# Performance work log

Hardware: AMD Instinct MI355X
Metric: run time of the kernel (lower is better)

## Reference

```python
import jax, jax.numpy as jnp
import numpy as np

N_NODES = 500000
N_EDGES = 4000000
IN_DIM = 2
HID = 8
N_ITERS = 3


def _edge_net(x, row, col, e1_w, e1_b, e2_w, e2_b):
    # bi = x[col], bo = x[row]; B = cat([bi, bo]) is detached in torch
    B = jax.lax.stop_gradient(jnp.concatenate([x[col], x[row]], axis=-1))  # [E, 2*F]
    h = jnp.tanh(B @ e1_w + e1_b)
    return jax.nn.sigmoid(h @ e2_w + e2_b)  # [E, 1]


def _node_net(x, row, col, edge_attr, n1_w, n1_b, n2_w, n2_b):
    e = jax.lax.stop_gradient(edge_attr)  # [E, 1], detached in torch
    bi = x[col] * e  # [E, F]
    bo = x[row] * e
    mi = jax.ops.segment_sum(bo, col, num_segments=N_NODES)  # scatter_add over col
    mo = jax.ops.segment_sum(bi, row, num_segments=N_NODES)  # scatter_add over row
    M = jax.lax.stop_gradient(jnp.concatenate([mi, mo, x], axis=-1))  # [N, 3*F]
    h = jnp.tanh(M @ n1_w + n1_b)
    return jnp.tanh(h @ n2_w + n2_b)  # [N, HID]


def setup_inputs() -> dict:
    key = jax.random.key(0)
    ks = jax.random.split(key, 12)
    F = IN_DIM + HID  # 10
    s = lambda fan_in: 1.0 / np.sqrt(fan_in)
    return {
        "x": jax.random.normal(ks[0], (N_NODES, IN_DIM), jnp.float32),
        "edge_index": jax.random.randint(ks[1], (2, N_EDGES), 0, N_NODES),
        "win_w": jax.random.uniform(ks[2], (IN_DIM, HID), jnp.float32, -s(IN_DIM), s(IN_DIM)),
        "win_b": jax.random.uniform(ks[3], (HID,), jnp.float32, -s(IN_DIM), s(IN_DIM)),
        "e1_w": jax.random.uniform(ks[4], (2 * F, HID), jnp.float32, -s(2 * F), s(2 * F)),
        "e1_b": jax.random.uniform(ks[5], (HID,), jnp.float32, -s(2 * F), s(2 * F)),
        "e2_w": jax.random.uniform(ks[6], (HID, 1), jnp.float32, -s(HID), s(HID)),
        "e2_b": jax.random.uniform(ks[7], (1,), jnp.float32, -s(HID), s(HID)),
        "n1_w": jax.random.uniform(ks[8], (3 * F, HID), jnp.float32, -s(3 * F), s(3 * F)),
        "n1_b": jax.random.uniform(ks[9], (HID,), jnp.float32, -s(3 * F), s(3 * F)),
        "n2_w": jax.random.uniform(ks[10], (HID, HID), jnp.float32, -s(HID), s(HID)),
        "n2_b": jax.random.uniform(ks[11], (HID,), jnp.float32, -s(HID), s(HID)),
    }


def reference(x, edge_index, win_w, win_b, e1_w, e1_b, e2_w, e2_b, n1_w, n1_b, n2_w, n2_b):
    row, col = edge_index[0], edge_index[1]
    X = x
    H = jnp.tanh(X @ win_w + win_b)  # input_network
    xcat = jnp.concatenate([H, X], axis=-1)  # [N, 10]
    for _ in range(N_ITERS):
        e = _edge_net(xcat, row, col, e1_w, e1_b, e2_w, e2_b)
        H = _node_net(xcat, row, col, e, n1_w, n1_b, n2_w, n2_b)
        xcat = jnp.concatenate([H, X], axis=-1)
    out = _edge_net(xcat, row, col, e1_w, e1_b, e2_w, e2_b)
    return out.squeeze(-1)  # [E]
```

## Files before the change

### kernel.cpp

```cpp
#include <hip/hip_runtime.h>
#include <hip/hip_fp16.h>
#include <math.h>

#define N_NODES 500000
#define N_EDGES 4000000
#define FDIM 10
#define HID 8

#define DSPACE (2 * N_NODES)
#define NB 512
#define BSHIFT 11
#define BMASK 2047
#define NB_USED ((DSPACE + BMASK) / 2048)

#define IN_BLOCKS ((N_NODES + 255) / 256)
#define ROWS_PAD (IN_BLOCKS * 256)
#define NODE_BLOCKS2 ((N_NODES + 127) / 128)

typedef _Float16 h2v __attribute__((ext_vector_type(2)));

__device__ __forceinline__ h2v u2h(unsigned x) {
    union { unsigned u; h2v h; } t; t.u = x; return t.h;
}
__device__ __forceinline__ unsigned packh2(float a, float b) {
    union { __half2 h; unsigned u; } t; t.h = __floats2half2_rn(a, b); return t.u;
}
__device__ __forceinline__ float rfl_f(float x) {
    return __int_as_float(__builtin_amdgcn_readfirstlane(__float_as_int(x)));
}
__device__ __forceinline__ unsigned rfl_u(unsigned x) {
    return (unsigned)__builtin_amdgcn_readfirstlane((int)x);
}

__device__ __forceinline__ int nt_ld_i(const int* p) { return __builtin_nontemporal_load(p); }

__device__ __forceinline__ float fast_tanh(float x) {
    float e = __builtin_amdgcn_exp2f(x * 2.885390082f);
    return 1.0f - 2.0f * __builtin_amdgcn_rcpf(e + 1.0f);
}
__device__ __forceinline__ float fast_sigmoid(float x) {
    float e = __builtin_amdgcn_exp2f(-1.442695041f * x);
    return __builtin_amdgcn_rcpf(1.0f + e);
}

__global__ __launch_bounds__(256) void input_kernel(const float* __restrict__ x,
                                                    const float* __restrict__ win_w,
                                                    const float* __restrict__ win_b,
                                                    uint4* __restrict__ xh,
                                                    unsigned* __restrict__ xs) {
    int n = blockIdx.x * 256 + threadIdx.x;
    float x0 = 0.f, x1 = 0.f;
    if (n < N_NODES) { x0 = x[2 * n]; x1 = x[2 * n + 1]; }
    float h[HID];
#pragma unroll
    for (int j = 0; j < HID; j++)
        h[j] = fast_tanh(x0 * win_w[j] + x1 * win_w[HID + j] + win_b[j]);
    xh[n] = make_uint4(packh2(h[0], h[1]), packh2(h[2], h[3]),
                       packh2(h[4], h[5]), packh2(h[6], h[7]));
    xs[n] = packh2(x0, x1);
}

__global__ void bucket_hist_kernel(const int* __restrict__ row,
                                   const int* __restrict__ col,
                                   int* __restrict__ g_cnt) {
    __shared__ int s_cnt[NB];
    int tid = threadIdx.x;
    for (int i = tid; i < NB; i += 256) s_cnt[i] = 0;
    __syncthreads();
    int base = blockIdx.x * 4096;
#pragma unroll
    for (int k = 0; k < 16; k++) {
        int e = base + k * 256 + tid;
        if (e < N_EDGES) {
            int c = nt_ld_i(col + e), r = nt_ld_i(row + e);
            atomicAdd(&s_cnt[(2 * c) >> BSHIFT], 1);
            atomicAdd(&s_cnt[(2 * r + 1) >> BSHIFT], 1);
        }
    }
    __syncthreads();
    for (int i = tid; i < NB; i += 256) {
        int v = s_cnt[i];
        if (v) atomicAdd(&g_cnt[i], v);
    }
}

__global__ void bucket_scan_kernel(const int* __restrict__ g_cnt,
                                   int* __restrict__ bucket_base,
                                   int* __restrict__ bucket_cur) {
    __shared__ int s[NB];
    int t = threadIdx.x;
    int c = g_cnt[t];
    s[t] = c;
    __syncthreads();
    for (int off = 1; off < NB; off <<= 1) {
        int v = (t >= off) ? s[t - off] : 0;
        __syncthreads();
        s[t] += v;
        __syncthreads();
    }
    int ex = s[t] - c;
    bucket_base[t] = ex;
    bucket_cur[t] = ex;
    if (t == NB - 1) bucket_base[NB] = s[t];
}

__global__ void bin_kernel(const int* __restrict__ row,
                           const int* __restrict__ col,
                           int* __restrict__ bucket_cur,
                           unsigned int* __restrict__ binned) {
    __shared__ int s_cnt[NB];
    __shared__ int s_start[NB];
    __shared__ int s_cur[NB];
    __shared__ int s_gbase[NB];
    __shared__ unsigned int s_items[8192];
    __shared__ unsigned short s_ibkt[8192];

    int tid = threadIdx.x;
    if (tid < NB) s_cnt[tid] = 0;
    __syncthreads();

    int base = blockIdx.x * 4096;
    int cc[4], rr[4];
#pragma unroll
    for (int k = 0; k < 4; k++) {
        int e = base + k * 1024 + tid;
        bool ok = (e < N_EDGES);
        cc[k] = ok ? nt_ld_i(col + e) : -1;
        rr[k] = ok ? nt_ld_i(row + e) : -1;
        if (ok) {
            atomicAdd(&s_cnt[(2 * cc[k]) >> BSHIFT], 1);
            atomicAdd(&s_cnt[(2 * rr[k] + 1) >> BSHIFT], 1);
        }
    }
    __syncthreads();

    if (tid < NB) s_start[tid] = s_cnt[tid];
    __syncthreads();
    for (int off = 1; off < NB; off <<= 1) {
        int v = 0;
        if (tid < NB && tid >= off) v = s_start[tid - off];
        __syncthreads();
        if (tid < NB) s_start[tid] += v;
        __syncthreads();
    }
    if (tid < NB) {
        int ex = s_start[tid] - s_cnt[tid];
        s_start[tid] = ex;
        s_cur[tid] = ex;
    }
    __syncthreads();

#pragma unroll
    for (int k = 0; k < 4; k++) {
        if (cc[k] >= 0) {
            int d0 = 2 * cc[k];
            int b0 = d0 >> BSHIFT;
            int s0 = atomicAdd(&s_cur[b0], 1);
            s_items[s0] = ((unsigned)(d0 & BMASK) << 19) | (unsigned)rr[k];
            s_ibkt[s0] = (unsigned short)b0;
            int d1 = 2 * rr[k] + 1;
            int b1 = d1 >> BSHIFT;
            int s1 = atomicAdd(&s_cur[b1], 1);
            s_items[s1] = ((unsigned)(d1 & BMASK) << 19) | (unsigned)cc[k];
            s_ibkt[s1] = (unsigned short)b1;
        }
    }
    __syncthreads();

    if (tid < NB) s_gbase[tid] = atomicAdd(&bucket_cur[tid], s_cnt[tid]);
    __syncthreads();

    int tot = s_start[NB - 1] + s_cnt[NB - 1];
    for (int s = tid; s < tot; s += 1024) {
        int b = s_ibkt[s];
        int g = s_gbase[b] + (s - s_start[b]);
        binned[g] = s_items[s];
    }
}

__global__ void csr_kernel(const unsigned int* __restrict__ binned,
                           const int* __restrict__ bucket_base,
                           int* __restrict__ offs,
                           int* __restrict__ entries) {
    __shared__ int s_deg[2048];
    __shared__ int s_cur[2048];
    __shared__ int s_pair[1024];

    int t = threadIdx.x;
    int b = blockIdx.x;
    if (b == 0 && t == 0) offs[DSPACE] = 2 * N_EDGES;

    int ebase = bucket_base[b];
    int eend = bucket_base[b + 1];

    s_deg[t] = 0;
    s_deg[t + 1024] = 0;
    __syncthreads();

    for (int p = ebase + t; p < eend; p += 1024)
        atomicAdd(&s_deg[binned[p] >> 19], 1);
    __syncthreads();

    int d0 = s_deg[2 * t], d1 = s_deg[2 * t + 1];
    s_pair[t] = d0 + d1;
    __syncthreads();
    for (int off = 1; off < 1024; off <<= 1) {
        int v = (t >= off) ? s_pair[t - off] : 0;
        __syncthreads();
        s_pair[t] += v;
        __syncthreads();
    }
    int pex = s_pair[t] - (d0 + d1);
    s_cur[2 * t] = pex;
    s_cur[2 * t + 1] = pex + d0;

    int dest0 = b * 2048 + 2 * t;
    if (dest0 < DSPACE) offs[dest0] = ebase + pex;
    if (dest0 + 1 < DSPACE) offs[dest0 + 1] = ebase + pex + d0;
    __syncthreads();

    for (int p = ebase + t; p < eend; p += 1024) {
        unsigned int it = binned[p];
        int dl = it >> 19;
        int other = it & 0x7FFFF;
        int pos = atomicAdd(&s_cur[dl], 1);
        entries[ebase + pos] = other;
    }
}

__global__ __launch_bounds__(256, 6) void node_kernel(
        const uint4* __restrict__ xh,
        const unsigned* __restrict__ xs,
        const int* __restrict__ offs,
        const int* __restrict__ entries,
        const float* __restrict__ e1_w,
        const float* __restrict__ e1_b,
        const float* __restrict__ e2_w,
        const float* __restrict__ e2_b,
        const float* __restrict__ n1_w,
        const float* __restrict__ n1_b,
        const float* __restrict__ n2_w,
        const float* __restrict__ n2_b,
        uint4* __restrict__ xh_next) {
    __shared__ uint4 s_wtop4[10];
    __shared__ uint4 s_wbot4[10];
    __shared__ float s_scal[17];
    __shared__ float s_n1w[30 * HID];
    __shared__ float s_n1b[HID];
    __shared__ float s_n2w[HID * HID];
    __shared__ float s_n2b[HID];
    __shared__ float s_mo[128 * 11];

    int tid = threadIdx.x;
    if (tid < 40) {
        int kk = tid >> 3, j = tid & 7;
        ((unsigned*)s_wtop4)[tid] = packh2(e1_w[(2 * kk) * HID + j],
                                           e1_w[(2 * kk + 1) * HID + j]);
        ((unsigned*)s_wbot4)[tid] = packh2(e1_w[(FDIM + 2 * kk) * HID + j],
                                           e1_w[(FDIM + 2 * kk + 1) * HID + j]);
    } else if (tid < 48) s_scal[tid - 40] = e1_b[tid - 40];
    else if (tid < 56) s_scal[tid - 40] = e2_w[tid - 48];
    else if (tid == 56) s_scal[16] = e2_b[0];
    if (tid < 240) s_n1w[tid] = n1_w[tid];
    else if (tid < 248) s_n1b[tid - 240] = n1_b[tid - 240];
    if (tid < 64) s_n2w[tid] = n2_w[tid];
    else if (tid < 72) s_n2b[tid - 64] = n2_b[tid - 64];
    __syncthreads();

    bool up = tid >= 128;
    int lt = up ? tid - 128 : tid;
    int n = blockIdx.x * 128 + lt;
    bool act = n < N_NODES;

    const uint4* selfw4 = up ? s_wbot4 : s_wtop4;
    const unsigned* othw = up ? (const unsigned*)s_wtop4 : (const unsigned*)s_wbot4;

    unsigned so[40];
#pragma unroll
    for (int i = 0; i < 40; i++) so[i] = rfl_u(othw[i]);
    float sb[HID], sv[HID];
#pragma unroll
    for (int j = 0; j < HID; j++) { sb[j] = rfl_f(s_scal[j]); sv[j] = rfl_f(s_scal[8 + j]); }
    float sc = rfl_f(s_scal[16]);

    unsigned xp[5] = {0, 0, 0, 0, 0};
    float m[FDIM];
#pragma unroll
    for (int k = 0; k < FDIM; k++) m[k] = 0.f;

    if (act) {
        uint4 xq = xh[n]; unsigned xx = xs[n];
        xp[0] = xq.x; xp[1] = xq.y; xp[2] = xq.z; xp[3] = xq.w; xp[4] = xx;

        float us[HID];
#pragma unroll
        for (int j = 0; j < HID; j++) us[j] = sb[j];
#pragma unroll
        for (int kk = 0; kk < 5; kk++) {
            uint4 wa = selfw4[2 * kk];
            uint4 wb = selfw4[2 * kk + 1];
            h2v a = u2h(xp[kk]);
            us[0] = __builtin_amdgcn_fdot2(a, u2h(wa.x), us[0], false);
            us[1] = __builtin_amdgcn_fdot2(a, u2h(wa.y), us[1], false);
            us[2] = __builtin_amdgcn_fdot2(a, u2h(wa.z), us[2], false);
            us[3] = __builtin_amdgcn_fdot2(a, u2h(wa.w), us[3], false);
            us[4] = __builtin_amdgcn_fdot2(a, u2h(wb.x), us[4], false);
            us[5] = __builtin_amdgcn_fdot2(a, u2h(wb.y), us[5], false);
            us[6] = __builtin_amdgcn_fdot2(a, u2h(wb.z), us[6], false);
            us[7] = __builtin_amdgcn_fdot2(a, u2h(wb.w), us[7], false);
        }

        int dest = 2 * n + (up ? 1 : 0);
        int p0 = nt_ld_i(offs + dest), p1 = nt_ld_i(offs + dest + 1);
        int np = p1 - p0;

        if (np > 0) {
            int o0 = entries[p0];
            uint4 A = xh[o0]; unsigned Ax = xs[o0];
            int i1 = (np > 1) ? p0 + 1 : p0;
            int o1 = entries[i1];
            uint4 B = xh[o1]; unsigned Bx = xs[o1];
            int i2 = (np > 2) ? p0 + 2 : i1;
            int o2 = entries[i2];

            for (int p = p0; p < p1; ++p) {
                int i3 = (p + 3 < p1) ? p + 3 : p1 - 1;
                int o3 = entries[i3];
                uint4 C = xh[o2]; unsigned Cx = xs[o2];

                unsigned cp[5] = { A.x, A.y, A.z, A.w, Ax };
                float acc[HID];
#pragma unroll
                for (int j = 0; j < HID; j++) acc[j] = us[j];
#pragma unroll
                for (int kk = 0; kk < 5; kk++) {
                    h2v a = u2h(cp[kk]);
#pragma unroll
                    for (int j = 0; j < HID; j++)
                        acc[j] = __builtin_amdgcn_fdot2(a, u2h(so[kk * 8 + j]), acc[j], false);
                }
                float d = sc;
#pragma unroll
                for (int j = 0; j < HID; j++) d += fast_tanh(acc[j]) * sv[j];
                float e = fast_sigmoid(d);
#pragma unroll
                for (int kk = 0; kk < 5; kk++) {
                    h2v a = u2h(cp[kk]);
                    m[2 * kk]     += e * (float)a.x;
                    m[2 * kk + 1] += e * (float)a.y;
                }
                A = B; Ax = Bx; B = C; Bx = Cx; o2 = o3;
            }
        }
    }

    if (up && act) {
        int lb = lt * 11;
#pragma unroll
        for (int k = 0; k < FDIM; k++) s_mo[lb + k] = m[k];
    }
    __syncthreads();

    if (!up && act) {
        int lb = lt * 11;
        float xn[FDIM];
#pragma unroll
        for (int kk = 0; kk < 5; kk++) {
            h2v a = u2h(xp[kk]);
            xn[2 * kk] = (float)a.x; xn[2 * kk + 1] = (float)a.y;
        }
        float h1[HID];
#pragma unroll
        for (int j = 0; j < HID; j++) h1[j] = s_n1b[j];
#pragma unroll
        for (int k = 0; k < FDIM; k++) {
            float mo_k = s_mo[lb + k];
#pragma unroll
            for (int j = 0; j < HID; j++) {
                h1[j] += m[k]  * s_n1w[k * HID + j];
                h1[j] += mo_k  * s_n1w[(FDIM + k) * HID + j];
                h1[j] += xn[k] * s_n1w[(2 * FDIM + k) * HID + j];
            }
        }
#pragma unroll
        for (int j = 0; j < HID; j++) h1[j] = fast_tanh(h1[j]);

        float H[HID];
#pragma unroll
        for (int j = 0; j < HID; j++) H[j] = s_n2b[j];
#pragma unroll
        for (int k = 0; k < HID; k++) {
#pragma unroll
            for (int j = 0; j < HID; j++) H[j] += h1[k] * s_n2w[k * HID + j];
        }
        xh_next[n] = make_uint4(packh2(fast_tanh(H[0]), fast_tanh(H[1])),
                                packh2(fast_tanh(H[2]), fast_tanh(H[3])),
                                packh2(fast_tanh(H[4]), fast_tanh(H[5])),
                                packh2(fast_tanh(H[6]), fast_tanh(H[7])));
    }
}

__global__ __launch_bounds__(256) void edge_kernel(const int* __restrict__ row,
                                                   const int* __restrict__ col,
                                                   const uint4* __restrict__ xh,
                                                   const unsigned* __restrict__ xs,
                                                   const float* __restrict__ e1_w,
                                                   const float* __restrict__ e1_b,
                                                   const float* __restrict__ e2_w,
                                                   const float* __restrict__ e2_b,
                                                   float* __restrict__ out) {
    __shared__ unsigned s_top[40];
    __shared__ uint4 s_bot4[10];
    __shared__ float s_scal[17];
    int tid = threadIdx.x;
    unsigned* s_bot = (unsigned*)s_bot4;
    if (tid < 40) {
        int kk = tid >> 3, j = tid & 7;
        s_top[tid] = packh2(e1_w[(2 * kk) * HID + j], e1_w[(2 * kk + 1) * HID + j]);
        s_bot[tid] = packh2(e1_w[(FDIM + 2 * kk) * HID + j], e1_w[(FDIM + 2 * kk + 1) * HID + j]);
    } else if (tid < 48) s_scal[tid - 40] = e1_b[tid - 40];
    else if (tid < 56) s_scal[tid - 40] = e2_w[tid - 48];
    else if (tid == 56) s_scal[16] = e2_b[0];
    __syncthreads();

    unsigned st[40];
#pragma unroll
    for (int i = 0; i < 40; i++) st[i] = rfl_u(s_top[i]);
    float sb[HID], sv[HID];
#pragma unroll
    for (int j = 0; j < HID; j++) { sb[j] = rfl_f(s_scal[j]); sv[j] = rfl_f(s_scal[8 + j]); }
    float sc = rfl_f(s_scal[16]);

    int i = blockIdx.x * 256 + tid;
    if (i >= N_EDGES) return;

    int r = nt_ld_i(row + i), c = nt_ld_i(col + i);
    uint4 aq = xh[c]; unsigned ax = xs[c];
    uint4 bq = xh[r]; unsigned bx = xs[r];
    unsigned ap[5] = { aq.x, aq.y, aq.z, aq.w, ax };
    unsigned bp[5] = { bq.x, bq.y, bq.z, bq.w, bx };

    float acc[HID];
#pragma unroll
    for (int j = 0; j < HID; j++) acc[j] = sb[j];
#pragma unroll
    for (int kk = 0; kk < 5; kk++) {
        h2v a = u2h(ap[kk]);
#pragma unroll
        for (int j = 0; j < HID; j++)
            acc[j] = __builtin_amdgcn_fdot2(a, u2h(st[kk * 8 + j]), acc[j], false);
    }
#pragma unroll
    for (int kk = 0; kk < 5; kk++) {
        uint4 wa = s_bot4[2 * kk];
        uint4 wb = s_bot4[2 * kk + 1];
        h2v b = u2h(bp[kk]);
        acc[0] = __builtin_amdgcn_fdot2(b, u2h(wa.x), acc[0], false);
        acc[1] = __builtin_amdgcn_fdot2(b, u2h(wa.y), acc[1], false);
        acc[2] = __builtin_amdgcn_fdot2(b, u2h(wa.z), acc[2], false);
        acc[3] = __builtin_amdgcn_fdot2(b, u2h(wa.w), acc[3], false);
        acc[4] = __builtin_amdgcn_fdot2(b, u2h(wb.x), acc[4], false);
        acc[5] = __builtin_amdgcn_fdot2(b, u2h(wb.y), acc[5], false);
        acc[6] = __builtin_amdgcn_fdot2(b, u2h(wb.z), acc[6], false);
        acc[7] = __builtin_amdgcn_fdot2(b, u2h(wb.w), acc[7], false);
    }

    float d = sc;
#pragma unroll
    for (int j = 0; j < HID; j++) d += fast_tanh(acc[j]) * sv[j];
    out[i] = fast_sigmoid(d);
}

extern "C" void kernel_launch(void* const* d_in, const int* in_sizes, int n_in,
                              void* d_out, int out_size, void* d_ws, size_t ws_size,
                              hipStream_t stream) {
    const float* x      = (const float*)d_in[0];
    const int*   eidx   = (const int*)d_in[1];
    const float* win_w  = (const float*)d_in[2];
    const float* win_b  = (const float*)d_in[3];
    const float* e1_w   = (const float*)d_in[4];
    const float* e1_b   = (const float*)d_in[5];
    const float* e2_w   = (const float*)d_in[6];
    const float* e2_b   = (const float*)d_in[7];
    const float* n1_w   = (const float*)d_in[8];
    const float* n1_b   = (const float*)d_in[9];
    const float* n2_w   = (const float*)d_in[10];
    const float* n2_b   = (const float*)d_in[11];
    float* out = (float*)d_out;

    const int* row = eidx;
    const int* col = eidx + N_EDGES;

    char* w = (char*)d_ws;
    uint4* xh0 = (uint4*)w;            w += (size_t)ROWS_PAD * 16;
    uint4* xh1 = (uint4*)w;            w += (size_t)ROWS_PAD * 16;
    unsigned* xs = (unsigned*)w;       w += (size_t)ROWS_PAD * 4;
    unsigned int* binned = (unsigned int*)w; w += (size_t)2 * N_EDGES * 4;
    int* entries = (int*)w;            w += (size_t)2 * N_EDGES * 4;
    int* offs = (int*)w;               w += (size_t)(DSPACE + 64) * 4;
    int* g_cnt = (int*)w;              w += NB * 4;
    int* bucket_base = (int*)w;        w += (NB + 64) * 4;
    int* bucket_cur = (int*)w;

    const int BLK = 256;
    int edge_blocks = (N_EDGES + BLK - 1) / BLK;
    int chunk_blocks = (N_EDGES + 4095) / 4096;

    hipMemsetAsync(g_cnt, 0, NB * sizeof(int), stream);
    bucket_hist_kernel<<<chunk_blocks, 256, 0, stream>>>(row, col, g_cnt);
    bucket_scan_kernel<<<1, NB, 0, stream>>>(g_cnt, bucket_base, bucket_cur);
    bin_kernel<<<chunk_blocks, 1024, 0, stream>>>(row, col, bucket_cur, binned);
    csr_kernel<<<NB_USED, 1024, 0, stream>>>(binned, bucket_base, offs, entries);

    input_kernel<<<IN_BLOCKS, BLK, 0, stream>>>(x, win_w, win_b, xh0, xs);

    uint4* cur = xh0;
    uint4* nxt = xh1;
    for (int it = 0; it < 3; it++) {
        node_kernel<<<NODE_BLOCKS2, BLK, 0, stream>>>(
            cur, xs, offs, entries, e1_w, e1_b, e2_w, e2_b,
            n1_w, n1_b, n2_w, n2_b, nxt);
        uint4* t = cur; cur = nxt; nxt = t;
    }

    edge_kernel<<<edge_blocks, BLK, 0, stream>>>(
        row, col, cur, xs, e1_w, e1_b, e2_w, e2_b, out);
}
```

Before: 984.8 us.

## Split neighbor lists into node-range phases for cache-blocked gathers in persistent node kernel

After: 989.4 us. About the same (+0.5%).

```diff
diff --git a/kernel.cpp b/kernel.cpp
--- a/kernel.cpp
+++ b/kernel.cpp
@@ -16,6 +16,9 @@
 #define IN_BLOCKS ((N_NODES + 255) / 256)
 #define ROWS_PAD (IN_BLOCKS * 256)
 #define NODE_BLOCKS2 ((N_NODES + 127) / 128)
+#define PGRID 1303
+#define NPH 4
+#define PHB 17
 
 typedef _Float16 h2v __attribute__((ext_vector_type(2)));
 
@@ -180,58 +183,65 @@
 
 __global__ void csr_kernel(const unsigned int* __restrict__ binned,
                            const int* __restrict__ bucket_base,
-                           int* __restrict__ offs,
+                           int* __restrict__ offs4,
                            int* __restrict__ entries) {
-    __shared__ int s_deg[2048];
-    __shared__ int s_cur[2048];
+    __shared__ int s_deg[2048 * NPH];
     __shared__ int s_pair[1024];
 
     int t = threadIdx.x;
     int b = blockIdx.x;
-    if (b == 0 && t == 0) offs[DSPACE] = 2 * N_EDGES;
 
     int ebase = bucket_base[b];
     int eend = bucket_base[b + 1];
 
-    s_deg[t] = 0;
-    s_deg[t + 1024] = 0;
-    __syncthreads();
-
-    for (int p = ebase + t; p < eend; p += 1024)
-        atomicAdd(&s_deg[binned[p] >> 19], 1);
-    __syncthreads();
-
-    int d0 = s_deg[2 * t], d1 = s_deg[2 * t + 1];
-    s_pair[t] = d0 + d1;
-    __syncthreads();
-    for (int off = 1; off < 1024; off <<= 1) {
-        int v = (t >= off) ? s_pair[t - off] : 0;
-        __syncthreads();
-        s_pair[t] += v;
-        __syncthreads();
-    }
-    int pex = s_pair[t] - (d0 + d1);
-    s_cur[2 * t] = pex;
-    s_cur[2 * t + 1] = pex + d0;
-
-    int dest0 = b * 2048 + 2 * t;
-    if (dest0 < DSPACE) offs[dest0] = ebase + pex;
-    if (dest0 + 1 < DSPACE) offs[dest0 + 1] = ebase + pex + d0;
+#pragma unroll
+    for (int i = 0; i < 2048 * NPH; i += 1024) s_deg[t + i] = 0;
     __syncthreads();
 
     for (int p = ebase + t; p < eend; p += 1024) {
         unsigned int it = binned[p];
         int dl = it >> 19;
-        int other = it & 0x7FFFF;
-        int pos = atomicAdd(&s_cur[dl], 1);
-        entries[ebase + pos] = other;
+        int o = it & 0x7FFFF;
+        atomicAdd(&s_deg[(dl << 2) | (o >> PHB)], 1);
+    }
+    __syncthreads();
+
+    int base8 = t * 8;
+    int sum = 0;
+#pragma unroll
+    for (int i = 0; i < 8; i++) sum += s_deg[base8 + i];
+    s_pair[t] = sum;
+    __syncthreads();
+    for (int off = 1; off < 1024; off <<= 1) {
+        int v = (t >= off) ? s_pair[t - off] : 0;
+        __syncthreads();
+        s_pair[t] += v;
+        __syncthreads();
+    }
+    int run = s_pair[t] - sum;
+    int gbase = b * (2048 * NPH) + base8;
+#pragma unroll
+    for (int i = 0; i < 8; i++) {
+        int d = s_deg[base8 + i];
+        s_deg[base8 + i] = run;
+        offs4[gbase + i] = ebase + run;
+        run += d;
+    }
+    __syncthreads();
+
+    for (int p = ebase + t; p < eend; p += 1024) {
+        unsigned int it = binned[p];
+        int dl = it >> 19;
+        int o = it & 0x7FFFF;
+        int pos = atomicAdd(&s_deg[(dl << 2) | (o >> PHB)], 1);
+        entries[ebase + pos] = o;
     }
 }
 
 __global__ __launch_bounds__(256, 6) void node_kernel(
         const uint4* __restrict__ xh,
         const unsigned* __restrict__ xs,
-        const int* __restrict__ offs,
+        const int* __restrict__ offs4,
         const int* __restrict__ entries,
         const float* __restrict__ e1_w,
         const float* __restrict__ e1_b,
@@ -269,8 +279,6 @@
 
     bool up = tid >= 128;
     int lt = up ? tid - 128 : tid;
-    int n = blockIdx.x * 128 + lt;
-    bool act = n < N_NODES;
 
     const uint4* selfw4 = up ? s_wbot4 : s_wtop4;
     const unsigned* othw = up ? (const unsigned*)s_wtop4 : (const unsigned*)s_wbot4;
@@ -283,120 +291,121 @@
     for (int j = 0; j < HID; j++) { sb[j] = rfl_f(s_scal[j]); sv[j] = rfl_f(s_scal[8 + j]); }
     float sc = rfl_f(s_scal[16]);
 
-    unsigned xp[5] = {0, 0, 0, 0, 0};
-    float m[FDIM];
-#pragma unroll
-    for (int k = 0; k < FDIM; k++) m[k] = 0.f;
-
-    if (act) {
-        uint4 xq = xh[n]; unsigned xx = xs[n];
-        xp[0] = xq.x; xp[1] = xq.y; xp[2] = xq.z; xp[3] = xq.w; xp[4] = xx;
-
+    for (int nb = blockIdx.x; nb < NODE_BLOCKS2; nb += PGRID) {
+        int n = nb * 128 + lt;
+        bool act = n < N_NODES;
+
+        unsigned xp[5] = {0, 0, 0, 0, 0};
+        float m[FDIM];
+#pragma unroll
+        for (int k = 0; k < FDIM; k++) m[k] = 0.f;
         float us[HID];
-#pragma unroll
-        for (int j = 0; j < HID; j++) us[j] = sb[j];
-#pragma unroll
-        for (int kk = 0; kk < 5; kk++) {
-            uint4 wa = selfw4[2 * kk];
-            uint4 wb = selfw4[2 * kk + 1];
-            h2v a = u2h(xp[kk]);
-            us[0] = __builtin_amdgcn_fdot2(a, u2h(wa.x), us[0], false);
-            us[1] = __builtin_amdgcn_fdot2(a, u2h(wa.y), us[1], false);
-            us[2] = __builtin_amdgcn_fdot2(a, u2h(wa.z), us[2], false);
-            us[3] = __builtin_amdgcn_fdot2(a, u2h(wa.w), us[3], false);
-            us[4] = __builtin_amdgcn_fdot2(a, u2h(wb.x), us[4], false);
-            us[5] = __builtin_amdgcn_fdot2(a, u2h(wb.y), us[5], false);
-            us[6] = __builtin_amdgcn_fdot2(a, u2h(wb.z), us[6], false);
-            us[7] = __builtin_amdgcn_fdot2(a, u2h(wb.w), us[7], false);
-        }
-
-        int dest = 2 * n + (up ? 1 : 0);
-        int p0 = nt_ld_i(offs + dest), p1 = nt_ld_i(offs + dest + 1);
-        int np = p1 - p0;
-
-        if (np > 0) {
-            int o0 = entries[p0];
-            uint4 A = xh[o0]; unsigned Ax = xs[o0];
-            int i1 = (np > 1) ? p0 + 1 : p0;
-            int o1 = entries[i1];
-            uint4 B = xh[o1]; unsigned Bx = xs[o1];
-            int i2 = (np > 2) ? p0 + 2 : i1;
-            int o2 = entries[i2];
-
-            for (int p = p0; p < p1; ++p) {
-                int i3 = (p + 3 < p1) ? p + 3 : p1 - 1;
-                int o3 = entries[i3];
-                uint4 C = xh[o2]; unsigned Cx = xs[o2];
-
-                unsigned cp[5] = { A.x, A.y, A.z, A.w, Ax };
-                float acc[HID];
-#pragma unroll
-                for (int j = 0; j < HID; j++) acc[j] = us[j];
-#pragma unroll
-                for (int kk = 0; kk < 5; kk++) {
-                    h2v a = u2h(cp[kk]);
-#pragma unroll
-                    for (int j = 0; j < HID; j++)
-                        acc[j] = __builtin_amdgcn_fdot2(a, u2h(so[kk * 8 + j]), acc[j], false);
+        int b4 = 0, ps = 0;
+
+        if (act) {
+            uint4 xq = xh[n]; unsigned xx = xs[n];
+            xp[0] = xq.x; xp[1] = xq.y; xp[2] = xq.z; xp[3] = xq.w; xp[4] = xx;
+
+#pragma unroll
+            for (int j = 0; j < HID; j++) us[j] = sb[j];
+#pragma unroll
+            for (int kk = 0; kk < 5; kk++) {
+                uint4 wa = selfw4[2 * kk];
+                uint4 wb = selfw4[2 * kk + 1];
+                h2v a = u2h(xp[kk]);
+                us[0] = __builtin_amdgcn_fdot2(a, u2h(wa.x), us[0], false);
+                us[1] = __builtin_amdgcn_fdot2(a, u2h(wa.y), us[1], false);
+                us[2] = __builtin_amdgcn_fdot2(a, u2h(wa.z), us[2], false);
+                us[3] = __builtin_amdgcn_fdot2(a, u2h(wa.w), us[3], false);
+                us[4] = __builtin_amdgcn_fdot2(a, u2h(wb.x), us[4], false);
+                us[5] = __builtin_amdgcn_fdot2(a, u2h(wb.y), us[5], false);
+                us[6] = __builtin_amdgcn_fdot2(a, u2h(wb.z), us[6], false);
+                us[7] = __builtin_amdgcn_fdot2(a, u2h(wb.w), us[7], false);
+            }
+
+            int dest = 2 * n + (up ? 1 : 0);
+            b4 = dest * 4;
+            ps = nt_ld_i(offs4 + b4);
+        }
+
+        for (int ph = 0; ph < NPH; ph++) {
+            if (act) {
+                int pe = nt_ld_i(offs4 + b4 + ph + 1);
+                for (int p = ps; p < pe; ++p) {
+                    int o = entries[p];
+                    uint4 cH = xh[o]; unsigned cX = xs[o];
+                    unsigned cp[5] = { cH.x, cH.y, cH.z, cH.w, cX };
+                    float acc[HID];
+#pragma unroll
+                    for (int j = 0; j < HID; j++) acc[j] = us[j];
+#pragma unroll
+                    for (int kk = 0; kk < 5; kk++) {
+                        h2v a = u2h(cp[kk]);
+#pragma unroll
+                        for (int j = 0; j < HID; j++)
+                            acc[j] = __builtin_amdgcn_fdot2(a, u2h(so[kk * 8 + j]), acc[j], false);
+                    }
+                    float d = sc;
+#pragma unroll
+                    for (int j = 0; j < HID; j++) d += fast_tanh(acc[j]) * sv[j];
+                    float e = fast_sigmoid(d);
+#pragma unroll
+                    for (int kk = 0; kk < 5; kk++) {
+                        h2v a = u2h(cp[kk]);
+                        m[2 * kk]     += e * (float)a.x;
+                        m[2 * kk + 1] += e * (float)a.y;
+                    }
                 }
-                float d = sc;
-#pragma unroll
-                for (int j = 0; j < HID; j++) d += fast_tanh(acc[j]) * sv[j];
-                float e = fast_sigmoid(d);
-#pragma unroll
-                for (int kk = 0; kk < 5; kk++) {
-                    h2v a = u2h(cp[kk]);
-                    m[2 * kk]     += e * (float)a.x;
-                    m[2 * kk + 1] += e * (float)a.y;
+                ps = pe;
+            }
+            __syncthreads();
+        }
+
+        if (up && act) {
+            int lb = lt * 11;
+#pragma unroll
+            for (int k = 0; k < FDIM; k++) s_mo[lb + k] = m[k];
+        }
+        __syncthreads();
+
+        if (!up && act) {
+            int lb = lt * 11;
+            float xn[FDIM];
+#pragma unroll
+            for (int kk = 0; kk < 5; kk++) {
+                h2v a = u2h(xp[kk]);
+                xn[2 * kk] = (float)a.x; xn[2 * kk + 1] = (float)a.y;
+            }
+            float h1[HID];
+#pragma unroll
+            for (int j = 0; j < HID; j++) h1[j] = s_n1b[j];
+#pragma unroll
+            for (int k = 0; k < FDIM; k++) {
+                float mo_k = s_mo[lb + k];
+#pragma unroll
+                for (int j = 0; j < HID; j++) {
+                    h1[j] += m[k]  * s_n1w[k * HID + j];
+                    h1[j] += mo_k  * s_n1w[(FDIM + k) * HID + j];
+                    h1[j] += xn[k] * s_n1w[(2 * FDIM + k) * HID + j];
                 }
-                A = B; Ax = Bx; B = C; Bx = Cx; o2 = o3;
             }
-        }
-    }
-
-    if (up && act) {
-        int lb = lt * 11;
-#pragma unroll
-        for (int k = 0; k < FDIM; k++) s_mo[lb + k] = m[k];
-    }
-    __syncthreads();
-
-    if (!up && act) {
-        int lb = lt * 11;
-        float xn[FDIM];
-#pragma unroll
-        for (int kk = 0; kk < 5; kk++) {
-            h2v a = u2h(xp[kk]);
-            xn[2 * kk] = (float)a.x; xn[2 * kk + 1] = (float)a.y;
-        }
-        float h1[HID];
-#pragma unroll
-        for (int j = 0; j < HID; j++) h1[j] = s_n1b[j];
-#pragma unroll
-        for (int k = 0; k < FDIM; k++) {
-            float mo_k = s_mo[lb + k];
-#pragma unroll
-            for (int j = 0; j < HID; j++) {
-                h1[j] += m[k]  * s_n1w[k * HID + j];
-                h1[j] += mo_k  * s_n1w[(FDIM + k) * HID + j];
-                h1[j] += xn[k] * s_n1w[(2 * FDIM + k) * HID + j];
+#pragma unroll
+            for (int j = 0; j < HID; j++) h1[j] = fast_tanh(h1[j]);
+
+            float H[HID];
+#pragma unroll
+            for (int j = 0; j < HID; j++) H[j] = s_n2b[j];
+#pragma unroll
+            for (int k = 0; k < HID; k++) {
+#pragma unroll
+                for (int j = 0; j < HID; j++) H[j] += h1[k] * s_n2w[k * HID + j];
             }
-        }
-#pragma unroll
-        for (int j = 0; j < HID; j++) h1[j] = fast_tanh(h1[j]);
-
-        float H[HID];
-#pragma unroll
-        for (int j = 0; j < HID; j++) H[j] = s_n2b[j];
-#pragma unroll
-        for (int k = 0; k < HID; k++) {
-#pragma unroll
-            for (int j = 0; j < HID; j++) H[j] += h1[k] * s_n2w[k * HID + j];
-        }
-        xh_next[n] = make_uint4(packh2(fast_tanh(H[0]), fast_tanh(H[1])),
-                                packh2(fast_tanh(H[2]), fast_tanh(H[3])),
-                                packh2(fast_tanh(H[4]), fast_tanh(H[5])),
-                                packh2(fast_tanh(H[6]), fast_tanh(H[7])));
+            xh_next[n] = make_uint4(packh2(fast_tanh(H[0]), fast_tanh(H[1])),
+                                    packh2(fast_tanh(H[2]), fast_tanh(H[3])),
+                                    packh2(fast_tanh(H[4]), fast_tanh(H[5])),
+                                    packh2(fast_tanh(H[6]), fast_tanh(H[7])));
+        }
+        __syncthreads();
     }
 }
 
@@ -497,7 +506,7 @@
     unsigned* xs = (unsigned*)w;       w += (size_t)ROWS_PAD * 4;
     unsigned int* binned = (unsigned int*)w; w += (size_t)2 * N_EDGES * 4;
     int* entries = (int*)w;            w += (size_t)2 * N_EDGES * 4;
-    int* offs = (int*)w;               w += (size_t)(DSPACE + 64) * 4;
+    int* offs4 = (int*)w;              w += ((size_t)NB_USED * 2048 * NPH + 64) * 4;
     int* g_cnt = (int*)w;              w += NB * 4;
     int* bucket_base = (int*)w;        w += (NB + 64) * 4;
     int* bucket_cur = (int*)w;
@@ -510,15 +519,15 @@
     bucket_hist_kernel<<<chunk_blocks, 256, 0, stream>>>(row, col, g_cnt);
     bucket_scan_kernel<<<1, NB, 0, stream>>>(g_cnt, bucket_base, bucket_cur);
     bin_kernel<<<chunk_blocks, 1024, 0, stream>>>(row, col, bucket_cur, binned);
-    csr_kernel<<<NB_USED, 1024, 0, stream>>>(binned, bucket_base, offs, entries);
+    csr_kernel<<<NB_USED, 1024, 0, stream>>>(binned, bucket_base, offs4, entries);
 
     input_kernel<<<IN_BLOCKS, BLK, 0, stream>>>(x, win_w, win_b, xh0, xs);
 
     uint4* cur = xh0;
     uint4* nxt = xh1;
     for (int it = 0; it < 3; it++) {
-        node_kernel<<<NODE_BLOCKS2, BLK, 0, stream>>>(
-            cur, xs, offs, entries, e1_w, e1_b, e2_w, e2_b,
+        node_kernel<<<PGRID, BLK, 0, stream>>>(
+            cur, xs, offs4, entries, e1_w, e1_b, e2_w, e2_b,
             n1_w, n1_b, n2_w, n2_b, nxt);
         uint4* t = cur; cur = nxt; nxt = t;
     }
```

## Process both in- and out-edge lists per node thread, dropping shared-memory merge

Applied to the files above, without the earlier changes.

New measurement: 1.327 ms. 34.7% more time.

```diff
diff --git a/kernel.cpp b/kernel.cpp
--- a/kernel.cpp
+++ b/kernel.cpp
@@ -15,7 +15,6 @@
 
 #define IN_BLOCKS ((N_NODES + 255) / 256)
 #define ROWS_PAD (IN_BLOCKS * 256)
-#define NODE_BLOCKS2 ((N_NODES + 127) / 128)
 
 typedef _Float16 h2v __attribute__((ext_vector_type(2)));
 
@@ -27,9 +26,6 @@
 }
 __device__ __forceinline__ float rfl_f(float x) {
     return __int_as_float(__builtin_amdgcn_readfirstlane(__float_as_int(x)));
-}
-__device__ __forceinline__ unsigned rfl_u(unsigned x) {
-    return (unsigned)__builtin_amdgcn_readfirstlane((int)x);
 }
 
 __device__ __forceinline__ int nt_ld_i(const int* p) { return __builtin_nontemporal_load(p); }
@@ -41,6 +37,33 @@
 __device__ __forceinline__ float fast_sigmoid(float x) {
     float e = __builtin_amdgcn_exp2f(-1.442695041f * x);
     return __builtin_amdgcn_rcpf(1.0f + e);
+}
+
+__device__ __forceinline__ float edge_sig(const uint4* __restrict__ wq,
+                                          const float* base,
+                                          const unsigned* cp,
+                                          const float* sv, float sc) {
+    float acc[HID];
+#pragma unroll
+    for (int j = 0; j < HID; j++) acc[j] = base[j];
+#pragma unroll
+    for (int kk = 0; kk < 5; kk++) {
+        uint4 wa = wq[2 * kk];
+        uint4 wb = wq[2 * kk + 1];
+        h2v a = u2h(cp[kk]);
+        acc[0] = __builtin_amdgcn_fdot2(a, u2h(wa.x), acc[0], false);
+        acc[1] = __builtin_amdgcn_fdot2(a, u2h(wa.y), acc[1], false);
+        acc[2] = __builtin_amdgcn_fdot2(a, u2h(wa.z), acc[2], false);
+        acc[3] = __builtin_amdgcn_fdot2(a, u2h(wa.w), acc[3], false);
+        acc[4] = __builtin_amdgcn_fdot2(a, u2h(wb.x), acc[4], false);
+        acc[5] = __builtin_amdgcn_fdot2(a, u2h(wb.y), acc[5], false);
+        acc[6] = __builtin_amdgcn_fdot2(a, u2h(wb.z), acc[6], false);
+        acc[7] = __builtin_amdgcn_fdot2(a, u2h(wb.w), acc[7], false);
+    }
+    float d = sc;
+#pragma unroll
+    for (int j = 0; j < HID; j++) d += fast_tanh(acc[j]) * sv[j];
+    return fast_sigmoid(d);
 }
 
 __global__ __launch_bounds__(256) void input_kernel(const float* __restrict__ x,
@@ -228,7 +251,7 @@
     }
 }
 
-__global__ __launch_bounds__(256, 6) void node_kernel(
+__global__ __launch_bounds__(256, 4) void node_kernel(
         const uint4* __restrict__ xh,
         const unsigned* __restrict__ xs,
         const int* __restrict__ offs,
@@ -242,127 +265,109 @@
         const float* __restrict__ n2_w,
         const float* __restrict__ n2_b,
         uint4* __restrict__ xh_next) {
-    __shared__ uint4 s_wtop4[10];
-    __shared__ uint4 s_wbot4[10];
+    __shared__ uint4 s_e4[20];
     __shared__ float s_scal[17];
     __shared__ float s_n1w[30 * HID];
     __shared__ float s_n1b[HID];
     __shared__ float s_n2w[HID * HID];
     __shared__ float s_n2b[HID];
-    __shared__ float s_mo[128 * 11];
 
     int tid = threadIdx.x;
-    if (tid < 40) {
+    if (tid < 80) {
         int kk = tid >> 3, j = tid & 7;
-        ((unsigned*)s_wtop4)[tid] = packh2(e1_w[(2 * kk) * HID + j],
-                                           e1_w[(2 * kk + 1) * HID + j]);
-        ((unsigned*)s_wbot4)[tid] = packh2(e1_w[(FDIM + 2 * kk) * HID + j],
-                                           e1_w[(FDIM + 2 * kk + 1) * HID + j]);
-    } else if (tid < 48) s_scal[tid - 40] = e1_b[tid - 40];
-    else if (tid < 56) s_scal[tid - 40] = e2_w[tid - 48];
-    else if (tid == 56) s_scal[16] = e2_b[0];
+        ((unsigned*)s_e4)[tid] = packh2(e1_w[(2 * kk) * HID + j],
+                                        e1_w[(2 * kk + 1) * HID + j]);
+    } else if (tid < 88) s_scal[tid - 80] = e1_b[tid - 80];
+    else if (tid < 96) s_scal[tid - 80] = e2_w[tid - 88];
+    else if (tid == 96) s_scal[16] = e2_b[0];
     if (tid < 240) s_n1w[tid] = n1_w[tid];
     else if (tid < 248) s_n1b[tid - 240] = n1_b[tid - 240];
     if (tid < 64) s_n2w[tid] = n2_w[tid];
     else if (tid < 72) s_n2b[tid - 64] = n2_b[tid - 64];
     __syncthreads();
 
-    bool up = tid >= 128;
-    int lt = up ? tid - 128 : tid;
-    int n = blockIdx.x * 128 + lt;
-    bool act = n < N_NODES;
-
-    const uint4* selfw4 = up ? s_wbot4 : s_wtop4;
-    const unsigned* othw = up ? (const unsigned*)s_wtop4 : (const unsigned*)s_wbot4;
-
-    unsigned so[40];
-#pragma unroll
-    for (int i = 0; i < 40; i++) so[i] = rfl_u(othw[i]);
     float sb[HID], sv[HID];
 #pragma unroll
     for (int j = 0; j < HID; j++) { sb[j] = rfl_f(s_scal[j]); sv[j] = rfl_f(s_scal[8 + j]); }
     float sc = rfl_f(s_scal[16]);
 
-    unsigned xp[5] = {0, 0, 0, 0, 0};
-    float m[FDIM];
-#pragma unroll
-    for (int k = 0; k < FDIM; k++) m[k] = 0.f;
-
+    int n = blockIdx.x * 256 + tid;
+    bool act = n < N_NODES;
+
+    uint4 xq = xh[n]; unsigned xx = xs[n];
+    unsigned xp[5] = { xq.x, xq.y, xq.z, xq.w, xx };
+
+    float us[HID], vs[HID];
+#pragma unroll
+    for (int j = 0; j < HID; j++) { us[j] = sb[j]; vs[j] = sb[j]; }
+#pragma unroll
+    for (int kk = 0; kk < 5; kk++) {
+        h2v a = u2h(xp[kk]);
+        uint4 wa = s_e4[2 * kk],      wb = s_e4[2 * kk + 1];
+        uint4 wc = s_e4[10 + 2 * kk], wd = s_e4[11 + 2 * kk];
+        us[0] = __builtin_amdgcn_fdot2(a, u2h(wa.x), us[0], false);
+        us[1] = __builtin_amdgcn_fdot2(a, u2h(wa.y), us[1], false);
+        us[2] = __builtin_amdgcn_fdot2(a, u2h(wa.z), us[2], false);
+        us[3] = __builtin_amdgcn_fdot2(a, u2h(wa.w), us[3], false);
+        us[4] = __builtin_amdgcn_fdot2(a, u2h(wb.x), us[4], false);
+        us[5] = __builtin_amdgcn_fdot2(a, u2h(wb.y), us[5], false);
+        us[6] = __builtin_amdgcn_fdot2(a, u2h(wb.z), us[6], false);
+        us[7] = __builtin_amdgcn_fdot2(a, u2h(wb.w), us[7], false);
+        vs[0] = __builtin_amdgcn_fdot2(a, u2h(wc.x), vs[0], false);
+        vs[1] = __builtin_amdgcn_fdot2(a, u2h(wc.y), vs[1], false);
+        vs[2] = __builtin_amdgcn_fdot2(a, u2h(wc.z), vs[2], false);
+        vs[3] = __builtin_amdgcn_fdot2(a, u2h(wc.w), vs[3], false);
+        vs[4] = __builtin_amdgcn_fdot2(a, u2h(wd.x), vs[4], false);
+        vs[5] = __builtin_amdgcn_fdot2(a, u2h(wd.y), vs[5], false);
+        vs[6] = __builtin_amdgcn_fdot2(a, u2h(wd.z), vs[6], false);
+        vs[7] = __builtin_amdgcn_fdot2(a, u2h(wd.w), vs[7], false);
+    }
+
+    int pa = 0, na = 0, pb = 0, nb = 0;
     if (act) {
-        uint4 xq = xh[n]; unsigned xx = xs[n];
-        xp[0] = xq.x; xp[1] = xq.y; xp[2] = xq.z; xp[3] = xq.w; xp[4] = xx;
-
-        float us[HID];
-#pragma unroll
-        for (int j = 0; j < HID; j++) us[j] = sb[j];
+        int o0 = nt_ld_i(offs + 2 * n);
+        int o1 = nt_ld_i(offs + 2 * n + 1);
+        int o2 = nt_ld_i(offs + 2 * n + 2);
+        pa = o0; na = o1 - o0;
+        pb = o1; nb = o2 - o1;
+    }
+
+    float mi[FDIM], mo[FDIM];
+#pragma unroll
+    for (int k = 0; k < FDIM; k++) { mi[k] = 0.f; mo[k] = 0.f; }
+
+    int len = na > nb ? na : nb;
+    for (int i = 0; i < len; ++i) {
+        bool va = i < na, vb = i < nb;
+        int ia = pa + (va ? i : 0);
+        int ib = pb + (vb ? i : 0);
+        int oa = entries[ia] & 0x7FFFF;
+        int ob = entries[ib] & 0x7FFFF;
+        uint4 Ha = xh[oa]; unsigned Xa = xs[oa];
+        uint4 Hb = xh[ob]; unsigned Xb = xs[ob];
+
+        unsigned ca[5] = { Ha.x, Ha.y, Ha.z, Ha.w, Xa };
+        float ea = edge_sig(s_e4 + 10, us, ca, sv, sc);
+        ea = va ? ea : 0.f;
 #pragma unroll
         for (int kk = 0; kk < 5; kk++) {
-            uint4 wa = selfw4[2 * kk];
-            uint4 wb = selfw4[2 * kk + 1];
-            h2v a = u2h(xp[kk]);
-            us[0] = __builtin_amdgcn_fdot2(a, u2h(wa.x), us[0], false);
-            us[1] = __builtin_amdgcn_fdot2(a, u2h(wa.y), us[1], false);
-            us[2] = __builtin_amdgcn_fdot2(a, u2h(wa.z), us[2], false);
-            us[3] = __builtin_amdgcn_fdot2(a, u2h(wa.w), us[3], false);
-            us[4] = __builtin_amdgcn_fdot2(a, u2h(wb.x), us[4], false);
-            us[5] = __builtin_amdgcn_fdot2(a, u2h(wb.y), us[5], false);
-            us[6] = __builtin_amdgcn_fdot2(a, u2h(wb.z), us[6], false);
-            us[7] = __builtin_amdgcn_fdot2(a, u2h(wb.w), us[7], false);
-        }
-
-        int dest = 2 * n + (up ? 1 : 0);
-        int p0 = nt_ld_i(offs + dest), p1 = nt_ld_i(offs + dest + 1);
-        int np = p1 - p0;
-
-        if (np > 0) {
-            int o0 = entries[p0];
-            uint4 A = xh[o0]; unsigned Ax = xs[o0];
-            int i1 = (np > 1) ? p0 + 1 : p0;
-            int o1 = entries[i1];
-            uint4 B = xh[o1]; unsigned Bx = xs[o1];
-            int i2 = (np > 2) ? p0 + 2 : i1;
-            int o2 = entries[i2];
-
-            for (int p = p0; p < p1; ++p) {
-                int i3 = (p + 3 < p1) ? p + 3 : p1 - 1;
-                int o3 = entries[i3];
-                uint4 C = xh[o2]; unsigned Cx = xs[o2];
-
-                unsigned cp[5] = { A.x, A.y, A.z, A.w, Ax };
-                float acc[HID];
-#pragma unroll
-                for (int j = 0; j < HID; j++) acc[j] = us[j];
-#pragma unroll
-                for (int kk = 0; kk < 5; kk++) {
-                    h2v a = u2h(cp[kk]);
-#pragma unroll
-                    for (int j = 0; j < HID; j++)
-                        acc[j] = __builtin_amdgcn_fdot2(a, u2h(so[kk * 8 + j]), acc[j], false);
-                }
-                float d = sc;
-#pragma unroll
-                for (int j = 0; j < HID; j++) d += fast_tanh(acc[j]) * sv[j];
-                float e = fast_sigmoid(d);
-#pragma unroll
-                for (int kk = 0; kk < 5; kk++) {
-                    h2v a = u2h(cp[kk]);
-                    m[2 * kk]     += e * (float)a.x;
-                    m[2 * kk + 1] += e * (float)a.y;
-                }
-                A = B; Ax = Bx; B = C; Bx = Cx; o2 = o3;
-            }
-        }
-    }
-
-    if (up && act) {
-        int lb = lt * 11;
-#pragma unroll
-        for (int k = 0; k < FDIM; k++) s_mo[lb + k] = m[k];
-    }
-    __syncthreads();
-
-    if (!up && act) {
-        int lb = lt * 11;
+            h2v a = u2h(ca[kk]);
+            mi[2 * kk]     += ea * (float)a.x;
+            mi[2 * kk + 1] += ea * (float)a.y;
+        }
+
+        unsigned cb[5] = { Hb.x, Hb.y, Hb.z, Hb.w, Xb };
+        float eb = edge_sig(s_e4, vs, cb, sv, sc);
+        eb = vb ? eb : 0.f;
+#pragma unroll
+        for (int kk = 0; kk < 5; kk++) {
+            h2v b = u2h(cb[kk]);
+            mo[2 * kk]     += eb * (float)b.x;
+            mo[2 * kk + 1] += eb * (float)b.y;
+        }
+    }
+
+    if (act) {
         float xn[FDIM];
 #pragma unroll
         for (int kk = 0; kk < 5; kk++) {
@@ -374,11 +379,10 @@
         for (int j = 0; j < HID; j++) h1[j] = s_n1b[j];
 #pragma unroll
         for (int k = 0; k < FDIM; k++) {
-            float mo_k = s_mo[lb + k];
 #pragma unroll
             for (int j = 0; j < HID; j++) {
-                h1[j] += m[k]  * s_n1w[k * HID + j];
-                h1[j] += mo_k  * s_n1w[(FDIM + k) * HID + j];
+                h1[j] += mi[k] * s_n1w[k * HID + j];
+                h1[j] += mo[k] * s_n1w[(FDIM + k) * HID + j];
                 h1[j] += xn[k] * s_n1w[(2 * FDIM + k) * HID + j];
             }
         }
@@ -409,23 +413,18 @@
                                                    const float* __restrict__ e2_w,
                                                    const float* __restrict__ e2_b,
                                                    float* __restrict__ out) {
-    __shared__ unsigned s_top[40];
-    __shared__ uint4 s_bot4[10];
+    __shared__ uint4 s_e4[20];
     __shared__ float s_scal[17];
     int tid = threadIdx.x;
-    unsigned* s_bot = (unsigned*)s_bot4;
-    if (tid < 40) {
+    if (tid < 80) {
         int kk = tid >> 3, j = tid & 7;
-        s_top[tid] = packh2(e1_w[(2 * kk) * HID + j], e1_w[(2 * kk + 1) * HID + j]);
-        s_bot[tid] = packh2(e1_w[(FDIM + 2 * kk) * HID + j], e1_w[(FDIM + 2 * kk + 1) * HID + j]);
-    } else if (tid < 48) s_scal[tid - 40] = e1_b[tid - 40];
-    else if (tid < 56) s_scal[tid - 40] = e2_w[tid - 48];
-    else if (tid == 56) s_scal[16] = e2_b[0];
-    __syncthreads();
-
-    unsigned st[40];
-#pragma unroll
-    for (int i = 0; i < 40; i++) st[i] = rfl_u(s_top[i]);
+        ((unsigned*)s_e4)[tid] = packh2(e1_w[(2 * kk) * HID + j],
+                                        e1_w[(2 * kk + 1) * HID + j]);
+    } else if (tid < 88) s_scal[tid - 80] = e1_b[tid - 80];
+    else if (tid < 96) s_scal[tid - 80] = e2_w[tid - 88];
+    else if (tid == 96) s_scal[16] = e2_b[0];
+    __syncthreads();
+
     float sb[HID], sv[HID];
 #pragma unroll
     for (int j = 0; j < HID; j++) { sb[j] = rfl_f(s_scal[j]); sv[j] = rfl_f(s_scal[8 + j]); }
@@ -445,15 +444,20 @@
     for (int j = 0; j < HID; j++) acc[j] = sb[j];
 #pragma unroll
     for (int kk = 0; kk < 5; kk++) {
+        uint4 wa = s_e4[2 * kk], wb = s_e4[2 * kk + 1];
         h2v a = u2h(ap[kk]);
-#pragma unroll
-        for (int j = 0; j < HID; j++)
-            acc[j] = __builtin_amdgcn_fdot2(a, u2h(st[kk * 8 + j]), acc[j], false);
+        acc[0] = __builtin_amdgcn_fdot2(a, u2h(wa.x), acc[0], false);
+        acc[1] = __builtin_amdgcn_fdot2(a, u2h(wa.y), acc[1], false);
+        acc[2] = __builtin_amdgcn_fdot2(a, u2h(wa.z), acc[2], false);
+        acc[3] = __builtin_amdgcn_fdot2(a, u2h(wa.w), acc[3], false);
+        acc[4] = __builtin_amdgcn_fdot2(a, u2h(wb.x), acc[4], false);
+        acc[5] = __builtin_amdgcn_fdot2(a, u2h(wb.y), acc[5], false);
+        acc[6] = __builtin_amdgcn_fdot2(a, u2h(wb.z), acc[6], false);
+        acc[7] = __builtin_amdgcn_fdot2(a, u2h(wb.w), acc[7], false);
     }
 #pragma unroll
     for (int kk = 0; kk < 5; kk++) {
-        uint4 wa = s_bot4[2 * kk];
-        uint4 wb = s_bot4[2 * kk + 1];
+        uint4 wa = s_e4[10 + 2 * kk], wb = s_e4[11 + 2 * kk];
         h2v b = u2h(bp[kk]);
         acc[0] = __builtin_amdgcn_fdot2(b, u2h(wa.x), acc[0], false);
         acc[1] = __builtin_amdgcn_fdot2(b, u2h(wa.y), acc[1], false);
@@ -496,7 +500,7 @@
     uint4* xh1 = (uint4*)w;            w += (size_t)ROWS_PAD * 16;
     unsigned* xs = (unsigned*)w;       w += (size_t)ROWS_PAD * 4;
     unsigned int* binned = (unsigned int*)w; w += (size_t)2 * N_EDGES * 4;
-    int* entries = (int*)w;            w += (size_t)2 * N_EDGES * 4;
+    int* entries = (int*)w;            w += ((size_t)2 * N_EDGES + 64) * 4;
     int* offs = (int*)w;               w += (size_t)(DSPACE + 64) * 4;
     int* g_cnt = (int*)w;              w += NB * 4;
     int* bucket_base = (int*)w;        w += (NB + 64) * 4;
@@ -517,7 +521,7 @@
     uint4* cur = xh0;
     uint4* nxt = xh1;
     for (int it = 0; it < 3; it++) {
-        node_kernel<<<NODE_BLOCKS2, BLK, 0, stream>>>(
+        node_kernel<<<IN_BLOCKS, BLK, 0, stream>>>(
             cur, xs, offs, entries, e1_w, e1_b, e2_w, e2_b,
             n1_w, n1_b, n2_w, n2_b, nxt);
         uint4* t = cur; cur = nxt; nxt = t;
```
